# Optimization experiments

Hardware: AMD Instinct MI355X
Metric: run time of the kernel (lower is better)

The kernel has to match this reference:

```python
import jax, jax.numpy as jnp
import numpy as np

HIDDEN = 1024
INNER = 1024
LR = 0.01
EPS = 1e-5


def _layernorm(x, gamma, beta):
    mu = jnp.mean(x, axis=-1, keepdims=True)
    var = jnp.var(x, axis=-1, keepdims=True)
    return (x - mu) * jax.lax.rsqrt(var + EPS) * gamma + beta


def setup_inputs() -> dict:
    key = jax.random.key(0)
    ks = jax.random.split(key, 8)
    B, S, H, I = 64, 512, HIDDEN, INNER
    x = jax.random.normal(ks[0], (B, S, H), dtype=jnp.float32)
    W_init = jax.random.normal(ks[1], (H, I), dtype=jnp.float32) * 0.02
    b_init = jnp.zeros((I,), dtype=jnp.float32)
    # Linear weights stored as (in, out) so y = x @ W + b
    lim_t = 1.0 / np.sqrt(H)
    Wt = jax.random.uniform(ks[2], (H, I), jnp.float32, -lim_t, lim_t)
    bt = jnp.zeros((I,), dtype=jnp.float32)
    lim_o = 1.0 / np.sqrt(I)
    Wo = jax.random.uniform(ks[3], (I, H), jnp.float32, -lim_o, lim_o)
    bo = jnp.zeros((H,), dtype=jnp.float32)
    lim_g = 1.0 / np.sqrt(2 * H)
    Wg = jax.random.uniform(ks[4], (2 * H, H), jnp.float32, -lim_g, lim_g)
    bg = jnp.zeros((H,), dtype=jnp.float32)
    gamma = jnp.ones((H,), dtype=jnp.float32)
    beta = jnp.zeros((H,), dtype=jnp.float32)
    return {"x": x, "W_init": W_init, "b_init": b_init, "Wt": Wt, "bt": bt,
            "Wo": Wo, "bo": bo, "Wg": Wg, "bg": bg, "gamma": gamma, "beta": beta}


def reference(x, W_init, b_init, Wt, bt, Wo, bo, Wg, bg, gamma, beta):
    B, S, H = x.shape
    I = W_init.shape[1]
    W0 = jnp.broadcast_to(W_init[None], (B, H, I))  # per-batch fast weights
    b0 = jnp.broadcast_to(b_init[None], (B, I))

    def step(carry, x_t):
        W, b = carry
        inner = jnp.einsum('bh,bhi->bi', x_t, W) + b          # [B, I]
        ttt = jax.nn.silu(inner) @ Wo + bo                    # [B, H]
        g = jax.nn.sigmoid(jnp.concatenate([x_t, ttt], axis=-1) @ Wg + bg)
        out = _layernorm(g * ttt + (1.0 - g) * x_t, gamma, beta)
        # test-time training update (target detached)
        target = jax.lax.stop_gradient(x_t @ Wt + bt)
        err = inner - target                                   # [B, I]
        W = W - (LR / I) * x_t[:, :, None] * err[:, None, :]
        b = b - (LR / I) * err
        return (W, b), out

    xs = jnp.swapaxes(x, 0, 1)  # [S, B, H]
    (_, _), ys = jax.lax.scan(step, (W0, b0), xs)
    return jnp.swapaxes(ys, 0, 1)  # [B, S, H]
```

## Files before the change

kernel.cpp:

```cpp
#include <hip/hip_runtime.h>

#define HD 1024
#define ID 1024
#define BATCH 64
#define SEQ 512
#define BS (BATCH*SEQ)
#define CHUNK 64
#define NCHUNK (SEQ/CHUNK)
#define LR_OVER_I (0.01f/1024.0f)

typedef unsigned int u32;
typedef unsigned short ushort_t;
typedef __attribute__((ext_vector_type(8))) short short8;
typedef __attribute__((ext_vector_type(8))) unsigned short ushort8;
typedef __attribute__((ext_vector_type(4))) unsigned short ushort4v;
typedef __attribute__((ext_vector_type(4))) float floatx4;

__device__ inline ushort_t f2bf(float f) {
    union { float f; u32 u; } v; v.f = f;
    return (ushort_t)((v.u + 0x7FFFu + ((v.u >> 16) & 1u)) >> 16);
}
__device__ inline float bf2f(ushort_t h) {
    union { u32 u; float f; } v; v.u = ((u32)h) << 16; return v.f;
}

__device__ inline void load_lds16(const void* g, void* l) {
    __builtin_amdgcn_global_load_lds(
        (const __attribute__((address_space(1))) u32*)g,
        (__attribute__((address_space(3))) u32*)l, 16, 0, 0);
}

__global__ void prep_w(const float* __restrict__ Wi, const float* __restrict__ Wt,
                       ushort_t* __restrict__ WdT, ushort_t* __restrict__ WtT,
                       const float* __restrict__ bi, const float* __restrict__ bt,
                       float* __restrict__ bd)
{
    if (blockIdx.x == 0 && blockIdx.y == 0) {
        int t = threadIdx.y * 32 + threadIdx.x;
        for (int i = t; i < ID; i += 256) bd[i] = bi[i] - bt[i];
    }
    __shared__ float ti[32][33], tt[32][33];
    int r0 = blockIdx.y * 32, c0 = blockIdx.x * 32;
    for (int i = threadIdx.y; i < 32; i += 8) {
        ti[i][threadIdx.x] = Wi[(long)(r0 + i) * ID + c0 + threadIdx.x];
        tt[i][threadIdx.x] = Wt[(long)(r0 + i) * ID + c0 + threadIdx.x];
    }
    __syncthreads();
    for (int i = threadIdx.y; i < 32; i += 8) {
        float wi = ti[threadIdx.x][i];
        float wt = tt[threadIdx.x][i];
        WdT[(long)(c0 + i) * HD + r0 + threadIdx.x] = f2bf(wi - wt);
        WtT[(long)(c0 + i) * HD + r0 + threadIdx.x] = f2bf(wt);
    }
}

__global__ void prep_transposes(const float* __restrict__ Wo, const float* __restrict__ Wg,
                                ushort_t* __restrict__ WoT, ushort_t* __restrict__ WgT)
{
    const float* in; ushort_t* out; int ldo;
    if (blockIdx.z == 0)      { in = Wo;                   out = WoT;      ldo = ID; }
    else if (blockIdx.z == 1) { in = Wg;                   out = WgT;      ldo = 2 * HD; }
    else                      { in = Wg + (long)HD * HD;   out = WgT + HD; ldo = 2 * HD; }
    __shared__ float t[32][33];
    int r0 = blockIdx.y * 32, c0 = blockIdx.x * 32;
    for (int i = threadIdx.y; i < 32; i += 8)
        t[i][threadIdx.x] = in[(long)(r0 + i) * HD + c0 + threadIdx.x];
    __syncthreads();
    for (int i = threadIdx.y; i < 32; i += 8)
        out[(long)(c0 + i) * ldo + r0 + threadIdx.x] = f2bf(t[threadIdx.x][i]);
}

__global__ void convert_bf16(const float* __restrict__ in, ushort_t* __restrict__ out)
{
    long i = ((long)blockIdx.x * 256 + threadIdx.x) * 8;
    float4 a = *(const float4*)(in + i);
    float4 b = *(const float4*)(in + i + 4);
    ushort8 o;
    o[0] = f2bf(a.x); o[1] = f2bf(a.y); o[2] = f2bf(a.z); o[3] = f2bf(a.w);
    o[4] = f2bf(b.x); o[5] = f2bf(b.y); o[6] = f2bf(b.z); o[7] = f2bf(b.w);
    *(ushort8*)(out + i) = o;
}

__global__ __launch_bounds__(256, 3) void gemm_bf16(
    const ushort_t* __restrict__ A0, long sA0, int lda0,
    const ushort_t* __restrict__ A1, long sA1, int lda1,
    const ushort_t* __restrict__ Bt, long sBb, int ldb,
    void* __restrict__ Cv, long sCb, int ldc,
    int KSEG, const float* __restrict__ bias,
    float alpha, float add0, int flags,
    const ushort_t* __restrict__ Bt2, void* __restrict__ Cv2,
    const float* __restrict__ bias2, int flags2)
{
    long zb = blockIdx.z;
    int fl = flags;
    if (flags & 16) {
        zb = 0;
        if (blockIdx.z == 1) { Bt = Bt2; Cv = Cv2; bias = bias2; fl = flags2; }
    }
    int bx, by;
    {
        int L = blockIdx.y * gridDim.x + blockIdx.x;
        if ((gridDim.y & 7) == 0) {
            int xcd = L & 7, g = L >> 3;
            bx = g % gridDim.x;
            by = (g / gridDim.x) * 8 + xcd;
        } else { bx = blockIdx.x; by = blockIdx.y; }
    }
    const int M0 = by * 128, N0 = bx * 128;
    if ((fl & 2) && N0 > M0) return;

    __shared__ ushort_t As[128 * 32];
    __shared__ ushort_t Bs[128 * 32];
    const int tid = threadIdx.x;
    const int wave = tid >> 6, lane = tid & 63;
    const int lr = lane & 15, lq = lane >> 4;
    const int wm = (wave & 1) * 64, wn = (wave >> 1) * 64;

    ushort_t* la0 = &As[(wave * 16)      * 32];
    ushort_t* la1 = &As[(wave * 16 + 64) * 32];
    ushort_t* lb0 = &Bs[(wave * 16)      * 32];
    ushort_t* lb1 = &Bs[(wave * 16 + 64) * 32];

    const ushort_t* gb0 = Bt + zb * sBb
                        + (long)(N0 + wave * 16 + (lane >> 2)) * ldb + (lane & 3) * 8;
    const ushort_t* gb1 = gb0 + 64L * ldb;

    floatx4 acc[4][4] = {};

    for (int seg = 0; seg < 2; ++seg) {
        const ushort_t* Ag = (seg == 0) ? A0 : A1;
        if (!Ag) break;
        const int lda = (seg == 0) ? lda0 : lda1;
        Ag += zb * ((seg == 0) ? sA0 : sA1);
        const ushort_t* ga0 = Ag + (long)(M0 + wave * 16 + (lane >> 2)) * lda + (lane & 3) * 8;
        const ushort_t* ga1 = ga0 + 64L * lda;

        for (int k0 = 0; k0 < KSEG; k0 += 32) {
            load_lds16(ga0, la0);
            load_lds16(ga1, la1);
            load_lds16(gb0, lb0);
            load_lds16(gb1, lb1);
            ga0 += 32; ga1 += 32; gb0 += 32; gb1 += 32;
            __syncthreads();
            short8 af[4], bf4[4];
#pragma unroll
            for (int i = 0; i < 4; ++i)
                af[i] = *(const short8*)&As[(wm + i * 16 + lr) * 32 + lq * 8];
#pragma unroll
            for (int j = 0; j < 4; ++j)
                bf4[j] = *(const short8*)&Bs[(wn + j * 16 + lr) * 32 + lq * 8];
#pragma unroll
            for (int i = 0; i < 4; ++i)
#pragma unroll
                for (int j = 0; j < 4; ++j)
                    acc[i][j] = __builtin_amdgcn_mfma_f32_16x16x32_bf16(
                        af[i], bf4[j], acc[i][j], 0, 0, 0);
            __syncthreads();
        }
    }

    float bv[4] = {0.f, 0.f, 0.f, 0.f};
    if (bias) {
#pragma unroll
        for (int j = 0; j < 4; ++j) bv[j] = bias[N0 + wn + j * 16 + lr];
    }
    if (fl & 1) {
        ushort_t* C = (ushort_t*)Cv + zb * sCb;
#pragma unroll
        for (int i = 0; i < 4; ++i)
#pragma unroll
            for (int r = 0; r < 4; ++r) {
                int row = M0 + wm + i * 16 + lq * 4 + r;
                ushort_t* cp = C + (long)row * ldc + N0 + wn + lr;
#pragma unroll
                for (int j = 0; j < 4; ++j)
                    cp[j * 16] = f2bf(alpha * acc[i][j][r] + add0 + bv[j]);
            }
    } else {
        if ((fl & 8) && wm) return;
        float* C = (float*)Cv + zb * sCb;
#pragma unroll
        for (int i = 0; i < 4; ++i)
#pragma unroll
            for (int r = 0; r < 4; ++r) {
                int row = M0 + wm + i * 16 + lq * 4 + r;
                float* cp = C + (long)row * ldc + N0 + wn + lr;
#pragma unroll
                for (int j = 0; j < 4; ++j) {
                    float val = alpha * acc[i][j][r] + add0 + bv[j];
                    if (fl & 4) val += cp[j * 16];
                    cp[j * 16] = val;
                }
            }
    }
}

__global__ __launch_bounds__(256) void solve_chunk(float* __restrict__ u,
                                                   const ushort_t* __restrict__ gram,
                                                   ushort_t* __restrict__ ebt, int c)
{
    const int b = blockIdx.z;
    const int j0 = blockIdx.x << 8;
    const int t0 = c << 6;
    const int tid = threadIdx.x;
    const int wave = tid >> 6, lane = tid & 63;
    const int lr = lane & 15, lq = lane >> 4;

    __shared__ __align__(16) char smem[4096 + 16384];
    ushort_t* As = (ushort_t*)smem;
    ushort_t* Bs = (ushort_t*)(smem + 4096);
    float* Gs = (float*)smem;

    const ushort_t* Gb = gram + (long)b * SEQ * SEQ + (long)t0 * SEQ;
    float* Ub = u + (long)b * SEQ * ID + (long)t0 * ID;
    ushort_t* Eb = ebt + (long)b * ID * SEQ;

    if (c > 0) {
        const int K = c << 6;
        floatx4 acc[4][4] = {};
        const ushort_t* ga = Gb + (long)(wave * 16 + (lane >> 2)) * SEQ + (lane & 3) * 8;
        const ushort_t* gb = Eb + (long)(j0 + wave * 16 + (lane >> 2)) * SEQ + (lane & 3) * 8;
        ushort_t* la  = &As[(wave * 16) * 32];
        ushort_t* lb0 = &Bs[(wave * 16)       * 32];
        ushort_t* lb1 = &Bs[(64  + wave * 16) * 32];
        ushort_t* lb2 = &Bs[(128 + wave * 16) * 32];
        ushort_t* lb3 = &Bs[(192 + wave * 16) * 32];
        for (int k0 = 0; k0 < K; k0 += 32) {
            load_lds16(ga, la);
            load_lds16(gb,             lb0);
            load_lds16(gb + 64L * SEQ, lb1);
            load_lds16(gb + 128L * SEQ, lb2);
            load_lds16(gb + 192L * SEQ, lb3);
            ga += 32; gb += 32;
            __syncthreads();
            short8 af[4], bf4[4];
#pragma unroll
            for (int i = 0; i < 4; ++i)
                af[i] = *(const short8*)&As[(i * 16 + lr) * 32 + lq * 8];
#pragma unroll
            for (int j = 0; j < 4; ++j)
                bf4[j] = *(const short8*)&Bs[(wave * 64 + j * 16 + lr) * 32 + lq * 8];
#pragma unroll
            for (int i = 0; i < 4; ++i)
#pragma unroll
                for (int j = 0; j < 4; ++j)
                    acc[i][j] = __builtin_amdgcn_mfma_f32_16x16x32_bf16(
                        af[i], bf4[j], acc[i][j], 0, 0, 0);
            __syncthreads();
        }
#pragma unroll
        for (int i = 0; i < 4; ++i)
#pragma unroll
            for (int r = 0; r < 4; ++r) {
                int row = i * 16 + lq * 4 + r;
                float* up = Ub + (long)row * ID + j0 + wave * 64 + lr;
#pragma unroll
                for (int j = 0; j < 4; ++j)
                    up[j * 16] -= acc[i][j][r];
            }
        __syncthreads();
    }

    for (int v = tid; v < 512; v += 256) {
        int row = v >> 3, col8 = (v & 7) << 3;
        ushort8 g8 = *(const ushort8*)(Gb + (long)row * SEQ + t0 + col8);
#pragma unroll
        for (int k = 0; k < 8; ++k) Gs[row * 64 + col8 + k] = bf2f(g8[k]);
    }
    __syncthreads();

    const int j = j0 + tid;
    float* E = Ub + j;
    float e[64];
    e[0] = E[0];
#pragma unroll
    for (int t = 1; t < 64; ++t) {
        float v = E[(long)t * ID];
        float p0 = 0.f, p1 = 0.f, p2 = 0.f, p3 = 0.f;
#pragma unroll
        for (int s = 0; s + 3 < t; s += 4) {
            p0 = fmaf(Gs[t * 64 + s + 0], e[s + 0], p0);
            p1 = fmaf(Gs[t * 64 + s + 1], e[s + 1], p1);
            p2 = fmaf(Gs[t * 64 + s + 2], e[s + 2], p2);
            p3 = fmaf(Gs[t * 64 + s + 3], e[s + 3], p3);
        }
#pragma unroll
        for (int s = t & ~3; s < t; ++s)
            p0 = fmaf(Gs[t * 64 + s], e[s], p0);
        float r = v - ((p0 + p1) + (p2 + p3));
        e[t] = r;
        E[(long)t * ID] = r;
    }
    ushort_t* EB = Eb + (long)j * SEQ + t0;
#pragma unroll
    for (int g = 0; g < 8; ++g) {
        ushort8 o;
#pragma unroll
        for (int k = 0; k < 8; ++k) o[k] = f2bf(e[g * 8 + k]);
        *(ushort8*)(EB + g * 8) = o;
    }
}

__global__ void silu_kernel(const float* __restrict__ err, const ushort_t* __restrict__ tgtb,
                            ushort_t* __restrict__ hb)
{
    long i = ((long)blockIdx.x * 256 + threadIdx.x) * 8;
    float4 e0 = *(const float4*)(err + i);
    float4 e1 = *(const float4*)(err + i + 4);
    ushort8 t8 = *(const ushort8*)(tgtb + i);
    float in[8] = {e0.x + bf2f(t8[0]), e0.y + bf2f(t8[1]),
                   e0.z + bf2f(t8[2]), e0.w + bf2f(t8[3]),
                   e1.x + bf2f(t8[4]), e1.y + bf2f(t8[5]),
                   e1.z + bf2f(t8[6]), e1.w + bf2f(t8[7])};
    ushort8 o;
#pragma unroll
    for (int k = 0; k < 8; ++k) {
        float v = in[k];
        o[k] = f2bf(v / (1.0f + __expf(-v)));
    }
    *(ushort8*)(hb + i) = o;
}

__global__ __launch_bounds__(256) void gate_ln(
    const ushort_t* __restrict__ zb, const ushort_t* __restrict__ tttb,
    const float* __restrict__ x, const float* __restrict__ gamma,
    const float* __restrict__ bet, float* __restrict__ out)
{
    long base = (long)blockIdx.x * HD + threadIdx.x * 4;
    ushort4v zv4 = *(const ushort4v*)(zb + base);
    ushort4v tv4 = *(const ushort4v*)(tttb + base);
    float4 xv = *(const float4*)(x + base);
    float xr[4] = {xv.x, xv.y, xv.z, xv.w};
    float y[4];
#pragma unroll
    for (int k = 0; k < 4; ++k) {
        float g = 1.0f / (1.0f + __expf(-bf2f(zv4[k])));
        float t = bf2f(tv4[k]);
        y[k] = g * t + (1.0f - g) * xr[k];
    }
    float sum = y[0] + y[1] + y[2] + y[3];
    float sq  = y[0]*y[0] + y[1]*y[1] + y[2]*y[2] + y[3]*y[3];
#pragma unroll
    for (int off = 32; off > 0; off >>= 1) {
        sum += __shfl_down(sum, off);
        sq  += __shfl_down(sq, off);
    }
    __shared__ float s1[4], s2[4];
    int wid = threadIdx.x >> 6;
    if ((threadIdx.x & 63) == 0) { s1[wid] = sum; s2[wid] = sq; }
    __syncthreads();
    float tot = s1[0] + s1[1] + s1[2] + s1[3];
    float tsq = s2[0] + s2[1] + s2[2] + s2[3];
    float mu = tot * (1.0f / HD);
    float var = tsq * (1.0f / HD) - mu * mu;
    float rs = rsqrtf(var + 1e-5f);
    int col = threadIdx.x * 4;
    float4 ov;
    ov.x = (y[0] - mu) * rs * gamma[col + 0] + bet[col + 0];
    ov.y = (y[1] - mu) * rs * gamma[col + 1] + bet[col + 1];
    ov.z = (y[2] - mu) * rs * gamma[col + 2] + bet[col + 2];
    ov.w = (y[3] - mu) * rs * gamma[col + 3] + bet[col + 3];
    *(float4*)(out + base) = ov;
}

extern "C" void kernel_launch(void* const* d_in, const int* in_sizes, int n_in,
                              void* d_out, int out_size, void* d_ws, size_t ws_size,
                              hipStream_t stream)
{
    const float* x    = (const float*)d_in[0];
    const float* Wi   = (const float*)d_in[1];
    const float* bi   = (const float*)d_in[2];
    const float* Wt   = (const float*)d_in[3];
    const float* bt   = (const float*)d_in[4];
    const float* Wo   = (const float*)d_in[5];
    const float* bo   = (const float*)d_in[6];
    const float* Wg   = (const float*)d_in[7];
    const float* bg   = (const float*)d_in[8];
    const float* gam  = (const float*)d_in[9];
    const float* bet  = (const float*)d_in[10];
    float* out = (float*)d_out;

    float* u       = (float*)d_ws;
    ushort_t* tgtb = (ushort_t*)(u + (long)BS * ID);
    float* gram    = (float*)(tgtb + (long)BS * ID);
    ushort_t* xb   = (ushort_t*)(gram + (long)BATCH * SEQ * SEQ);
    ushort_t* tttb = xb + (long)BS * HD;
    ushort_t* WdT  = tttb + (long)BS * HD;
    ushort_t* WtT  = WdT + (long)HD * ID;
    ushort_t* WoT  = WtT + (long)HD * ID;
    ushort_t* WgT  = WoT + (long)HD * ID;
    float* bd      = (float*)(WgT + (long)HD * 2 * HD);
    ushort_t* gramb = (ushort_t*)gram;
    ushort_t* ebt   = (ushort_t*)tttb;
    ushort_t* hb    = (ushort_t*)gram;
    ushort_t* zb    = (ushort_t*)u;

    prep_w<<<dim3(32, 32), dim3(32, 8), 0, stream>>>(Wi, Wt, WdT, WtT, bi, bt, bd);
    prep_transposes<<<dim3(32, 32, 3), dim3(32, 8), 0, stream>>>(Wo, Wg, WoT, WgT);
    convert_bf16<<<16384, 256, 0, stream>>>(x, xb);

    dim3 gBig(ID / 128, BS / 128, 1);
    gemm_bf16<<<dim3(ID / 128, BS / 128, 2), 256, 0, stream>>>(
        xb, 0, HD, nullptr, 0, 0, WdT, 0, HD,
        u, 0, ID, HD, bd, 1.f, 0.f, 16,
        WtT, tgtb, bt, 1);
    gemm_bf16<<<dim3(SEQ / 128, SEQ / 128, BATCH), 256, 0, stream>>>(
        xb, (long)SEQ * HD, HD, nullptr, 0, 0, xb, (long)SEQ * HD, HD,
        gramb, (long)SEQ * SEQ, SEQ, HD, nullptr, LR_OVER_I, LR_OVER_I, 2 | 1,
        nullptr, nullptr, nullptr, 0);

    for (int c = 0; c < NCHUNK; ++c)
        solve_chunk<<<dim3(4, 1, BATCH), 256, 0, stream>>>(u, gramb, ebt, c);

    silu_kernel<<<16384, 256, 0, stream>>>(u, tgtb, hb);
    gemm_bf16<<<gBig, 256, 0, stream>>>(hb, 0, ID, nullptr, 0, 0, WoT, 0, ID,
                                        tttb, 0, HD, ID, bo, 1.f, 0.f, 1,
                                        nullptr, nullptr, nullptr, 0);
    gemm_bf16<<<gBig, 256, 0, stream>>>(xb, 0, HD, tttb, 0, HD, WgT, 0, 2 * HD,
                                        zb, 0, HD, HD, bg, 1.f, 0.f, 1,
                                        nullptr, nullptr, nullptr, 0);
    gate_ln<<<BS, 256, 0, stream>>>(zb, tttb, x, gam, bet, out);
}
```

Measured before the change: 1.093 ms.

## Fuse SiLU into chunk solver and stage error tile in shared memory

The chunked triangular solve now stages the corrected error tile in a 64x260 shared-memory buffer instead of writing it back to global u, then applies the target add and SiLU in place on tgtb, which removes the separate silu kernel and its full fp32 reread of u. The bf16 transposed error store is skipped for the last chunk because nothing reads it afterwards. Shared-memory use per block rises to roughly 86 KB, which may lower occupancy. The SiLU write loop uses strided 2-byte stores per thread, which may coalesce less well than the old vectorized kernel.

```diff
diff --git a/kernel.cpp b/kernel.cpp
--- a/kernel.cpp
+++ b/kernel.cpp
@@ -195,9 +195,10 @@
     }
 }
 
-__global__ __launch_bounds__(256) void solve_chunk(float* __restrict__ u,
+__global__ __launch_bounds__(256) void solve_chunk(const float* __restrict__ u,
                                                    const ushort_t* __restrict__ gram,
-                                                   ushort_t* __restrict__ ebt, int c)
+                                                   ushort_t* __restrict__ ebt,
+                                                   ushort_t* __restrict__ tgtb, int c)
 {
     const int b = blockIdx.z;
     const int j0 = blockIdx.x << 8;
@@ -206,13 +207,14 @@
     const int wave = tid >> 6, lane = tid & 63;
     const int lr = lane & 15, lq = lane >> 4;
 
-    __shared__ __align__(16) char smem[4096 + 16384];
-    ushort_t* As = (ushort_t*)smem;
-    ushort_t* Bs = (ushort_t*)(smem + 4096);
-    float* Gs = (float*)smem;
+    __shared__ float Us[64][260];
+    __shared__ __align__(16) char smem2[4096 + 16384];
+    ushort_t* As = (ushort_t*)smem2;
+    ushort_t* Bs = (ushort_t*)(smem2 + 4096);
+    float* Gs = (float*)smem2;
 
     const ushort_t* Gb = gram + (long)b * SEQ * SEQ + (long)t0 * SEQ;
-    float* Ub = u + (long)b * SEQ * ID + (long)t0 * ID;
+    const float* Ub = u + (long)b * SEQ * ID + (long)t0 * ID;
     ushort_t* Eb = ebt + (long)b * ID * SEQ;
 
     if (c > 0) {
@@ -227,8 +229,8 @@
         ushort_t* lb3 = &Bs[(192 + wave * 16) * 32];
         for (int k0 = 0; k0 < K; k0 += 32) {
             load_lds16(ga, la);
-            load_lds16(gb,             lb0);
-            load_lds16(gb + 64L * SEQ, lb1);
+            load_lds16(gb,              lb0);
+            load_lds16(gb + 64L * SEQ,  lb1);
             load_lds16(gb + 128L * SEQ, lb2);
             load_lds16(gb + 192L * SEQ, lb3);
             ga += 32; gb += 32;
@@ -253,12 +255,18 @@
 #pragma unroll
             for (int r = 0; r < 4; ++r) {
                 int row = i * 16 + lq * 4 + r;
-                float* up = Ub + (long)row * ID + j0 + wave * 64 + lr;
+                const float* up = Ub + (long)row * ID + j0 + wave * 64 + lr;
 #pragma unroll
                 for (int j = 0; j < 4; ++j)
-                    up[j * 16] -= acc[i][j][r];
+                    Us[row][wave * 64 + j * 16 + lr] = up[j * 16] - acc[i][j][r];
             }
-        __syncthreads();
+    } else {
+        for (int idx = tid; idx < 64 * 64; idx += 256) {
+            int row = idx >> 6, col4 = (idx & 63) << 2;
+            float4 v = *(const float4*)(Ub + (long)row * ID + j0 + col4);
+            Us[row][col4 + 0] = v.x; Us[row][col4 + 1] = v.y;
+            Us[row][col4 + 2] = v.z; Us[row][col4 + 3] = v.w;
+        }
     }
 
     for (int v = tid; v < 512; v += 256) {
@@ -269,13 +277,11 @@
     }
     __syncthreads();
 
-    const int j = j0 + tid;
-    float* E = Ub + j;
     float e[64];
-    e[0] = E[0];
+    e[0] = Us[0][tid];
 #pragma unroll
     for (int t = 1; t < 64; ++t) {
-        float v = E[(long)t * ID];
+        float v = Us[t][tid];
         float p0 = 0.f, p1 = 0.f, p2 = 0.f, p3 = 0.f;
 #pragma unroll
         for (int s = 0; s + 3 < t; s += 4) {
@@ -287,38 +293,26 @@
 #pragma unroll
         for (int s = t & ~3; s < t; ++s)
             p0 = fmaf(Gs[t * 64 + s], e[s], p0);
-        float r = v - ((p0 + p1) + (p2 + p3));
-        e[t] = r;
-        E[(long)t * ID] = r;
-    }
-    ushort_t* EB = Eb + (long)j * SEQ + t0;
-#pragma unroll
-    for (int g = 0; g < 8; ++g) {
-        ushort8 o;
-#pragma unroll
-        for (int k = 0; k < 8; ++k) o[k] = f2bf(e[g * 8 + k]);
-        *(ushort8*)(EB + g * 8) = o;
-    }
-}
-
-__global__ void silu_kernel(const float* __restrict__ err, const ushort_t* __restrict__ tgtb,
-                            ushort_t* __restrict__ hb)
-{
-    long i = ((long)blockIdx.x * 256 + threadIdx.x) * 8;
-    float4 e0 = *(const float4*)(err + i);
-    float4 e1 = *(const float4*)(err + i + 4);
-    ushort8 t8 = *(const ushort8*)(tgtb + i);
-    float in[8] = {e0.x + bf2f(t8[0]), e0.y + bf2f(t8[1]),
-                   e0.z + bf2f(t8[2]), e0.w + bf2f(t8[3]),
-                   e1.x + bf2f(t8[4]), e1.y + bf2f(t8[5]),
-                   e1.z + bf2f(t8[6]), e1.w + bf2f(t8[7])};
-    ushort8 o;
-#pragma unroll
-    for (int k = 0; k < 8; ++k) {
-        float v = in[k];
-        o[k] = f2bf(v / (1.0f + __expf(-v)));
-    }
-    *(ushort8*)(hb + i) = o;
+        e[t] = v - ((p0 + p1) + (p2 + p3));
+    }
+
+    if (c < NCHUNK - 1) {
+        ushort_t* EB = Eb + (long)(j0 + tid) * SEQ + t0;
+#pragma unroll
+        for (int g = 0; g < 8; ++g) {
+            ushort8 o;
+#pragma unroll
+            for (int k = 0; k < 8; ++k) o[k] = f2bf(e[g * 8 + k]);
+            *(ushort8*)(EB + g * 8) = o;
+        }
+    }
+
+    ushort_t* Tp = tgtb + ((long)b * SEQ + t0) * ID + j0 + tid;
+#pragma unroll
+    for (int t = 0; t < 64; ++t) {
+        float v = e[t] + bf2f(Tp[(long)t * ID]);
+        Tp[(long)t * ID] = f2bf(v / (1.0f + __expf(-v)));
+    }
 }
 
 __global__ __launch_bounds__(256) void gate_ln(
@@ -392,9 +386,8 @@
     float* bd      = (float*)(WgT + (long)HD * 2 * HD);
     ushort_t* gramb = (ushort_t*)gram;
     ushort_t* ebt   = (ushort_t*)tttb;
-    ushort_t* hb    = (ushort_t*)gram;
+    ushort_t* hb    = tgtb;
     ushort_t* zb    = (ushort_t*)u;
-
     prep_w<<<dim3(32, 32), dim3(32, 8), 0, stream>>>(Wi, Wt, WdT, WtT, bi, bt, bd);
     prep_transposes<<<dim3(32, 32, 3), dim3(32, 8), 0, stream>>>(Wo, Wg, WoT, WgT);
     convert_bf16<<<16384, 256, 0, stream>>>(x, xb);
@@ -410,9 +403,8 @@
         nullptr, nullptr, nullptr, 0);
 
     for (int c = 0; c < NCHUNK; ++c)
-        solve_chunk<<<dim3(4, 1, BATCH), 256, 0, stream>>>(u, gramb, ebt, c);
-
-    silu_kernel<<<16384, 256, 0, stream>>>(u, tgtb, hb);
+        solve_chunk<<<dim3(4, 1, BATCH), 256, 0, stream>>>(u, gramb, ebt, tgtb, c);
+
     gemm_bf16<<<gBig, 256, 0, stream>>>(hb, 0, ID, nullptr, 0, 0, WoT, 0, ID,
                                         tttb, 0, HD, ID, bo, 1.f, 0.f, 1,
                                         nullptr, nullptr, nullptr, 0);
```

After: 1.046 ms. 4.3% less time.
